# Optimization experiments

Measured on AMD Instinct MI355X. Metric: run time of the kernel, lower is better.

Reference implementation:

```python
import jax, jax.numpy as jnp
import numpy as np

N = 50000
E = 800000
IN_C = 128
HEADS = 2
OUT_C = 64
NEG_SLOPE = 0.2  # PyG GATConv leaky_relu slope


def setup_inputs() -> dict:
    key = jax.random.key(0)
    ks = jax.random.split(key, 12)
    glorot = lambda k, shape: jax.random.normal(k, shape, jnp.float32) * np.sqrt(2.0 / (shape[0] + shape[-1]))
    return {
        "node_h": jax.random.normal(ks[0], (N, IN_C), jnp.float32),
        "edge_index_pc": jax.random.randint(ks[1], (2, E), 0, N, jnp.int64),
        "edge_index_mc": jax.random.randint(ks[2], (2, E), 0, N, jnp.int64),
        "W_pc": glorot(ks[3], (IN_C, HEADS * OUT_C)),
        "att_src_pc": glorot(ks[4], (HEADS, OUT_C)),
        "att_dst_pc": glorot(ks[5], (HEADS, OUT_C)),
        "bias_pc": jnp.zeros((HEADS * OUT_C,), jnp.float32),
        "W_mc": glorot(ks[6], (IN_C, HEADS * OUT_C)),
        "att_src_mc": glorot(ks[7], (HEADS, OUT_C)),
        "att_dst_mc": glorot(ks[8], (HEADS, OUT_C)),
        "bias_mc": jnp.zeros((HEADS * OUT_C,), jnp.float32),
    }


def _gat_conv(x, edge_index, W, att_src, att_dst, bias):
    # PyG GATConv (concat=True). x: [N, in], edge_index: [2, E] (src -> dst).
    n = x.shape[0]
    H, C = att_src.shape
    xw = (x @ W).reshape(n, H, C)                      # [N, H, C]
    a_src = jnp.sum(xw * att_src, axis=-1)             # [N, H]
    a_dst = jnp.sum(xw * att_dst, axis=-1)             # [N, H]
    src, dst = edge_index[0], edge_index[1]
    e = jax.nn.leaky_relu(a_src[src] + a_dst[dst], negative_slope=NEG_SLOPE)  # [E, H]
    # segment softmax over edges sharing the same destination node
    m = jax.ops.segment_max(e, dst, num_segments=n)    # [N, H]
    m = jnp.where(jnp.isfinite(m), m, 0.0)             # guard isolated nodes
    ex = jnp.exp(e - m[dst])
    denom = jax.ops.segment_sum(ex, dst, num_segments=n)
    alpha = ex / (denom[dst] + 1e-16)                  # [E, H]
    msg = xw[src] * alpha[:, :, None]                  # [E, H, C]
    out = jax.ops.segment_sum(msg, dst, num_segments=n)  # [N, H, C]
    return out.reshape(n, H * C) + bias


def reference(node_h, edge_index_pc, edge_index_mc,
              W_pc, att_src_pc, att_dst_pc, bias_pc,
              W_mc, att_src_mc, att_dst_mc, bias_mc):
    # eval mode: F.dropout and GATConv attention dropout are identity
    h_pc = jax.nn.elu(_gat_conv(node_h, edge_index_pc, W_pc, att_src_pc, att_dst_pc, bias_pc))
    h_mc = jax.nn.elu(_gat_conv(node_h, edge_index_mc, W_mc, att_src_mc, att_dst_mc, bias_mc))
    return (h_pc + h_mc) * 0.5
```

## Files before the change

### kernel.cpp

```cpp
#include <hip/hip_runtime.h>
#include <hip/hip_bf16.h>

#define IN_C   128
#define HC     128
#define OUT_C  64
#define EPB    4096
#define NBMAX  1024
#define CAP    3072

typedef short bf16x8 __attribute__((ext_vector_type(8)));
typedef float f32x4  __attribute__((ext_vector_type(4)));

__device__ __forceinline__ unsigned short f2bf(float f) {
    unsigned u = __float_as_uint(f);
    return (unsigned short)((u + 0x7FFF + ((u >> 16) & 1)) >> 16);
}

__device__ __forceinline__ void fma8(float* acc, float al, uint4 v) {
    acc[0] += al * __uint_as_float(v.x << 16);
    acc[1] += al * __uint_as_float(v.x & 0xFFFF0000u);
    acc[2] += al * __uint_as_float(v.y << 16);
    acc[3] += al * __uint_as_float(v.y & 0xFFFF0000u);
    acc[4] += al * __uint_as_float(v.z << 16);
    acc[5] += al * __uint_as_float(v.z & 0xFFFF0000u);
    acc[6] += al * __uint_as_float(v.w << 16);
    acc[7] += al * __uint_as_float(v.w & 0xFFFF0000u);
}

__global__ void k_detect(const void* __restrict__ h,
                         const void* __restrict__ e1,
                         const void* __restrict__ e2,
                         int* __restrict__ flags)
{
    if (blockIdx.x == 0 && threadIdx.x == 0) {
        const unsigned short* u = (const unsigned short*)h;
        int f32 = 0;
        for (int k = 0; k < 512; ++k) {
            int ex = (u[k] >> 7) & 0xFF;
            if (ex >= 0xE0) { f32 = 1; break; }
        }
        flags[0] = f32;
        const int* a = (const int*)e1;
        const int* b = (const int*)e2;
        int any1 = 0, any2 = 0;
        for (int k = 0; k < 64; ++k) { any1 |= a[2*k+1]; any2 |= b[2*k+1]; }
        flags[1] = (any1 == 0);
        flags[2] = (any2 == 0);
        flags[3] = 0;
    }
}

__device__ __forceinline__ float ldf(const void* p, int i, int f32) {
    if (f32) return ((const float*)p)[i];
    return __bfloat162float(((const __hip_bfloat16*)p)[i]);
}

__device__ __forceinline__ void load_edge(const void* ei, int e, int E, int i64,
                                          int& s, int& d)
{
    if (i64) {
        s = (int)((const long long*)ei)[e];
        d = (int)((const long long*)ei)[E + e];
    } else {
        s = ((const int*)ei)[e];
        d = ((const int*)ei)[E + e];
    }
}

__global__ void k_fill_sentinel(float* out, int total, float v)
{
    int i = blockIdx.x * blockDim.x + threadIdx.x;
    if (i < total) out[i] = v;
}

__global__ __launch_bounds__(256)
void k_prep(const void* __restrict__ Wpc, const void* __restrict__ Wmc,
            const int* __restrict__ flags,
            unsigned short* __restrict__ WTpc, unsigned short* __restrict__ WTmc)
{
    int idx = blockIdx.x * 256 + threadIdx.x;
    if (idx >= 2 * IN_C * HC) return;
    int conv = idx >= IN_C * HC;
    int r = idx - conv * IN_C * HC;
    int k = r >> 7, j = r & 127;
    float v = ldf(conv ? Wmc : Wpc, r, flags[0]);
    (conv ? WTmc : WTpc)[(size_t)j * IN_C + k] = f2bf(v);
}

__global__ __launch_bounds__(256)
void k_gs(const void* __restrict__ h,
          const unsigned short* __restrict__ WT0,
          const unsigned short* __restrict__ WT1,
          const void* __restrict__ atS0, const void* __restrict__ atD0,
          const void* __restrict__ atS1, const void* __restrict__ atD1,
          const int* __restrict__ flags,
          unsigned short* __restrict__ xw0, unsigned short* __restrict__ xw1,
          float* __restrict__ oas0, float* __restrict__ oad0,
          float* __restrict__ oas1, float* __restrict__ oad1,
          int n, int blocksG,
          const void* __restrict__ e1, const void* __restrict__ e2, int E,
          int NB, int blocksB,
          int* __restrict__ gcur1, int* __restrict__ gcur2,
          unsigned* __restrict__ bkt1, unsigned* __restrict__ bkt2)
{
    __shared__ int sh[2 * NBMAX];
    int tid = threadIdx.x;

    if (blockIdx.y < 2) {
        if ((int)blockIdx.x >= blocksG) return;
        int conv = blockIdx.y;
        const unsigned short* WT = conv ? WT1 : WT0;
        const void* atS = conv ? atS1 : atS0;
        const void* atD = conv ? atD1 : atD0;
        unsigned short* xw = conv ? xw1 : xw0;
        float* oaS = conv ? oas1 : oas0;
        float* oaD = conv ? oad1 : oad0;

        int wave = tid >> 6, lane = tid & 63;
        int cl = lane & 15, grp = lane >> 4;
        int base = blockIdx.x * 64 + wave * 16;
        int f32 = flags[0];

        int nodeLoad = base + cl;
        int nl = nodeLoad < n ? nodeLoad : (n - 1);
        bf16x8 afr[4];
        #pragma unroll
        for (int s = 0; s < 4; ++s) {
            int k0 = 32 * s + 8 * grp;
            if (f32) {
                const float4* hr = (const float4*)((const float*)h + (size_t)nl * IN_C + k0);
                float4 u0 = hr[0], u1 = hr[1];
                afr[s][0] = (short)f2bf(u0.x); afr[s][1] = (short)f2bf(u0.y);
                afr[s][2] = (short)f2bf(u0.z); afr[s][3] = (short)f2bf(u0.w);
                afr[s][4] = (short)f2bf(u1.x); afr[s][5] = (short)f2bf(u1.y);
                afr[s][6] = (short)f2bf(u1.z); afr[s][7] = (short)f2bf(u1.w);
            } else {
                afr[s] = *(const bf16x8*)((const unsigned short*)h + (size_t)nl * IN_C + k0);
            }
        }

        float vs_[4][2] = {{0.f,0.f},{0.f,0.f},{0.f,0.f},{0.f,0.f}};
        float vd_[4][2] = {{0.f,0.f},{0.f,0.f},{0.f,0.f},{0.f,0.f}};

        #pragma unroll
        for (int t = 0; t < 8; ++t) {
            int col = t * 16 + cl;
            f32x4 acc = {0.f, 0.f, 0.f, 0.f};
            #pragma unroll
            for (int s = 0; s < 4; ++s) {
                int k0 = 32 * s + 8 * grp;
                bf16x8 b = *(const bf16x8*)(WT + (size_t)col * IN_C + k0);
                acc = __builtin_amdgcn_mfma_f32_16x16x32_bf16(afr[s], b, acc, 0, 0, 0);
            }
            float aS = ldf(atS, col, f32);
            float aD = ldf(atD, col, f32);
            int hd = t >> 2;
            #pragma unroll
            for (int r = 0; r < 4; ++r) {
                int nodeOut = base + 4 * grp + r;
                float v = acc[r];
                if (nodeOut < n) xw[(size_t)nodeOut * HC + col] = f2bf(v);
                vs_[r][hd] += v * aS;
                vd_[r][hd] += v * aD;
            }
        }
        #pragma unroll
        for (int r = 0; r < 4; ++r) {
            #pragma unroll
            for (int hd = 0; hd < 2; ++hd) {
                float vs = vs_[r][hd], vd = vd_[r][hd];
                #pragma unroll
                for (int off = 1; off < 16; off <<= 1) {
                    vs += __shfl_xor(vs, off);
                    vd += __shfl_xor(vd, off);
                }
                int nodeOut = base + 4 * grp + r;
                if (cl == 0 && nodeOut < n) {
                    oaS[nodeOut * 2 + hd] = vs;
                    oaD[nodeOut * 2 + hd] = vd;
                }
            }
        }
    } else {
        if ((int)blockIdx.x >= blocksB) return;
        int conv = blockIdx.y - 2;
        const void* ei = conv ? e2 : e1;
        int* gcur = conv ? gcur2 : gcur1;
        unsigned* bkt = conv ? bkt2 : bkt1;
        int* cnt = sh;
        int* lbase = sh + NBMAX;
        for (int i = tid; i < NB; i += 256) cnt[i] = 0;
        __syncthreads();
        int base = blockIdx.x * EPB;
        int i64 = flags[1 + conv];
        int ss[EPB / 256], dd[EPB / 256];
        #pragma unroll
        for (int k = 0; k < EPB / 256; ++k) {
            int e = base + k * 256 + tid;
            if (e < E) {
                int s, d; load_edge(ei, e, E, i64, s, d);
                ss[k] = s; dd[k] = d;
                atomicAdd(&cnt[d >> 7], 1);
            } else dd[k] = -1;
        }
        __syncthreads();
        for (int i = tid; i < NB; i += 256) {
            int c = cnt[i];
            lbase[i] = c ? atomicAdd(&gcur[i], c) : 0;
            cnt[i] = 0;
        }
        __syncthreads();
        #pragma unroll
        for (int k = 0; k < EPB / 256; ++k) {
            if (dd[k] >= 0) {
                int b = dd[k] >> 7;
                int pos = lbase[b] + atomicAdd(&cnt[b], 1);
                if (pos < CAP)
                    bkt[(size_t)b * CAP + pos] =
                        ((unsigned)(dd[k] & 127) << 17) | (unsigned)ss[k];
            }
        }
    }
}

__global__ __launch_bounds__(256)
void k_bcsr4(unsigned* __restrict__ bkt1, unsigned* __restrict__ bkt2,
             unsigned* __restrict__ alp1, unsigned* __restrict__ alp2,
             const int* __restrict__ gcur1, const int* __restrict__ gcur2,
             const float* __restrict__ as1, const float* __restrict__ ad1,
             const float* __restrict__ as2, const float* __restrict__ ad2,
             int2* __restrict__ rs1, int2* __restrict__ rs2,
             int NB, int n)
{
    __shared__ unsigned ebuf[CAP];
    __shared__ float sc0[CAP];
    __shared__ float sc1[CAP];
    __shared__ int cnt[128], off[128], exc[128];
    int conv = blockIdx.y;
    unsigned* seg = (conv ? bkt2 : bkt1) + (size_t)blockIdx.x * CAP;
    unsigned* alp = (conv ? alp2 : alp1) + (size_t)blockIdx.x * CAP;
    const int* gcur = conv ? gcur2 : gcur1;
    const float2* asv = (const float2*)(conv ? as2 : as1);
    const float2* adv = (const float2*)(conv ? ad2 : ad1);
    int2* rs = conv ? rs2 : rs1;
    int b = blockIdx.x, tid = threadIdx.x;
    int nb0 = b << 7;
    int nd = n - nb0; if (nd > 128) nd = 128;
    int cntE = gcur[b]; if (cntE > CAP) cntE = CAP;

    for (int i = tid; i < cntE; i += 256) ebuf[i] = seg[i];
    if (tid < 128) cnt[tid] = 0;
    __syncthreads();
    for (int i = tid; i < cntE; i += 256)
        atomicAdd(&cnt[ebuf[i] >> 17], 1);
    __syncthreads();
    int v = (tid < 128) ? cnt[tid] : 0;
    if (tid < 128) off[tid] = v;
    __syncthreads();
    for (int o = 1; o < 128; o <<= 1) {
        int x = (tid < 128 && tid >= o) ? off[tid - o] : 0;
        __syncthreads();
        if (tid < 128) off[tid] += x;
        __syncthreads();
    }
    if (tid < 128) exc[tid] = off[tid] - v;
    if (tid < nd) {
        int begA = b * CAP + exc[tid];
        rs[nb0 + tid] = make_int2(begA, begA + v);
    }
    if (tid < 128) cnt[tid] = 0;
    __syncthreads();
    for (int i = tid; i < cntE; i += 256) {
        unsigned pv = ebuf[i];
        int d = pv >> 17;
        int pos = atomicAdd(&cnt[d], 1);
        seg[exc[d] + pos] = pv & 0x1FFFFu;
    }
    __syncthreads();

    int d = tid >> 1, sub = tid & 1;
    int rc = (d < nd) ? cnt[d] : 0;
    int rb = exc[d];
    float2 ad = (d < nd) ? adv[nb0 + d] : make_float2(0.f, 0.f);
    float m0 = -1e30f, m1 = -1e30f;
    for (int i = sub; i < rc; i += 2) {
        int s = (int)seg[rb + i];
        float2 as = asv[s];
        float e0 = as.x + ad.x; e0 = e0 > 0.f ? e0 : 0.2f * e0;
        float e1 = as.y + ad.y; e1 = e1 > 0.f ? e1 : 0.2f * e1;
        sc0[rb + i] = e0; sc1[rb + i] = e1;
        m0 = fmaxf(m0, e0); m1 = fmaxf(m1, e1);
    }
    m0 = fmaxf(m0, __shfl_xor(m0, 1));
    m1 = fmaxf(m1, __shfl_xor(m1, 1));
    float s0 = 0.f, s1 = 0.f;
    for (int i = sub; i < rc; i += 2) {
        float ex0 = expf(sc0[rb + i] - m0);
        float ex1 = expf(sc1[rb + i] - m1);
        sc0[rb + i] = ex0; sc1[rb + i] = ex1;
        s0 += ex0; s1 += ex1;
    }
    s0 += __shfl_xor(s0, 1);
    s1 += __shfl_xor(s1, 1);
    float inv0 = 1.f / (s0 + 1e-16f), inv1 = 1.f / (s1 + 1e-16f);
    for (int i = sub; i < rc; i += 2) {
        unsigned a = (unsigned)f2bf(sc0[rb + i] * inv0)
                   | ((unsigned)f2bf(sc1[rb + i] * inv1) << 16);
        alp[rb + i] = a;
    }
}

__global__ __launch_bounds__(256)
void k_node11(const int2* __restrict__ rs1, const int2* __restrict__ rs2,
              const unsigned* __restrict__ csr1, const unsigned* __restrict__ csr2,
              const unsigned* __restrict__ alp1, const unsigned* __restrict__ alp2,
              const unsigned short* __restrict__ xw1, const unsigned short* __restrict__ xw2,
              const void* __restrict__ bias1, const void* __restrict__ bias2,
              const int* __restrict__ flags,
              float* __restrict__ out, int n)
{
    int tid = threadIdx.x;
    int nl = tid >> 4;
    int l  = tid & 15;
    int node = blockIdx.x * 16 + nl;
    if (node >= n) return;
    int f32 = flags[0];
    unsigned lofs = (unsigned)(l << 4);
    int c0 = l * 8;
    int hi = (l >= 8);
    float vv0[8];

    #pragma unroll
    for (int conv = 0; conv < 2; ++conv) {
        const int2* rs = conv ? rs2 : rs1;
        const unsigned* csr = conv ? csr2 : csr1;
        const unsigned* alp = conv ? alp2 : alp1;
        const char* xwb = (const char*)(conv ? xw2 : xw1);
        const void* bias = conv ? bias2 : bias1;

        int2 r = rs[node];
        int beg = r.x, deg = r.y - r.x;

        float acc[8] = {0.f,0.f,0.f,0.f,0.f,0.f,0.f,0.f};
        int t = 0;
        for (; t + 4 <= deg; t += 4) {
            unsigned sA = csr[beg + t],     sB = csr[beg + t + 1];
            unsigned sC = csr[beg + t + 2], sD = csr[beg + t + 3];
            unsigned aA = alp[beg + t],     aB = alp[beg + t + 1];
            unsigned aC = alp[beg + t + 2], aD = alp[beg + t + 3];
            uint4 vA = *(const uint4*)(xwb + (sA << 8) + lofs);
            uint4 vB = *(const uint4*)(xwb + (sB << 8) + lofs);
            uint4 vC = *(const uint4*)(xwb + (sC << 8) + lofs);
            uint4 vD = *(const uint4*)(xwb + (sD << 8) + lofs);
            float alA = __uint_as_float(hi ? (aA & 0xFFFF0000u) : (aA << 16));
            float alB = __uint_as_float(hi ? (aB & 0xFFFF0000u) : (aB << 16));
            float alC = __uint_as_float(hi ? (aC & 0xFFFF0000u) : (aC << 16));
            float alD = __uint_as_float(hi ? (aD & 0xFFFF0000u) : (aD << 16));
            fma8(acc, alA, vA);
            fma8(acc, alB, vB);
            fma8(acc, alC, vC);
            fma8(acc, alD, vD);
        }
        for (; t < deg; ++t) {
            unsigned s = csr[beg + t];
            unsigned a = alp[beg + t];
            float al = __uint_as_float(hi ? (a & 0xFFFF0000u) : (a << 16));
            uint4 v = *(const uint4*)(xwb + (s << 8) + lofs);
            fma8(acc, al, v);
        }

        if (conv == 0) {
            #pragma unroll
            for (int j = 0; j < 8; ++j) {
                float v = acc[j] + ldf(bias, c0 + j, f32);
                vv0[j] = v > 0.f ? v : expf(v) - 1.f;
            }
        } else {
            float vv1[8];
            #pragma unroll
            for (int j = 0; j < 8; ++j) {
                float v = acc[j] + ldf(bias, c0 + j, f32);
                vv1[j] = v > 0.f ? v : expf(v) - 1.f;
            }
            float4* o4 = (float4*)(out + (size_t)node * HC + c0);
            o4[0] = make_float4(0.5f * (vv0[0] + vv1[0]), 0.5f * (vv0[1] + vv1[1]),
                                0.5f * (vv0[2] + vv1[2]), 0.5f * (vv0[3] + vv1[3]));
            o4[1] = make_float4(0.5f * (vv0[4] + vv1[4]), 0.5f * (vv0[5] + vv1[5]),
                                0.5f * (vv0[6] + vv1[6]), 0.5f * (vv0[7] + vv1[7]));
        }
    }
}

static inline char* align64(char* p) {
    return (char*)(((size_t)p + 63) & ~(size_t)63);
}

extern "C" void kernel_launch(void* const* d_in, const int* in_sizes, int n_in,
                              void* d_out, int out_size, void* d_ws, size_t ws_size,
                              hipStream_t stream)
{
    const void* node_h = d_in[0];
    const void* ei_pc  = d_in[1];
    const void* ei_mc  = d_in[2];
    const void* W_pc   = d_in[3];
    const void* as_pc  = d_in[4];
    const void* ad_pc  = d_in[5];
    const void* b_pc   = d_in[6];
    const void* W_mc   = d_in[7];
    const void* as_mc  = d_in[8];
    const void* ad_mc  = d_in[9];
    const void* b_mc   = d_in[10];

    const int N = in_sizes[0] / IN_C;
    const int E = in_sizes[1] / 2;
    const int total = N * HC;
    const int NB = (N + 127) >> 7;
    float* out = (float*)d_out;
    const int fillBlocks = (out_size + 255) / 256;

    char* p = (char*)d_ws;
    int* flags = (int*)p;                       p += 256;
    unsigned short* WT_pc = (unsigned short*)p; p += (size_t)IN_C * HC * 2;
    unsigned short* WT_mc = (unsigned short*)p; p += (size_t)IN_C * HC * 2;
    unsigned short* xw_pc = (unsigned short*)p; p += (size_t)total * 2;
    unsigned short* xw_mc = (unsigned short*)p; p += (size_t)total * 2;
    float* aspc = (float*)p;                    p += (size_t)N * 2 * 4;
    float* adpc = (float*)p;                    p += (size_t)N * 2 * 4;
    float* asmc = (float*)p;                    p += (size_t)N * 2 * 4;
    float* admc = (float*)p;                    p += (size_t)N * 2 * 4;
    char* zbase = p;
    int* gcur1 = (int*)p;                       p += (size_t)NBMAX * 4;
    int* gcur2 = (int*)p;                       p += (size_t)NBMAX * 4;
    size_t zbytes = (size_t)(p - zbase);
    p = align64(p);
    int2* rs1 = (int2*)p;                       p += (size_t)N * 8;  p = align64(p);
    int2* rs2 = (int2*)p;                       p += (size_t)N * 8;  p = align64(p);
    unsigned* bkt1 = (unsigned*)p;              p += (size_t)NB * CAP * 4;
    unsigned* bkt2 = (unsigned*)p;              p += (size_t)NB * CAP * 4;
    unsigned* alp1 = (unsigned*)p;              p += (size_t)NB * CAP * 4;
    unsigned* alp2 = (unsigned*)p;              p += (size_t)NB * CAP * 4;

    {
        float sentinel = 0.f;
        if (n_in < 11) sentinel = 690.f;
        else if (in_sizes[1] != in_sizes[2]) sentinel = 702.f;
        else if (in_sizes[3] != IN_C * HC)   sentinel = 703.f;
        else if (in_sizes[7] != IN_C * HC)   sentinel = 707.f;
        else if (out_size != total)          sentinel = 720.f;
        else if (NB > NBMAX)                 sentinel = 730.f;
        else if (N >= (1 << 17))             sentinel = 741.f;
        size_t need = (size_t)(p - (char*)d_ws);
        if (sentinel == 0.f && ws_size < need) sentinel = 555.f;
        if (sentinel != 0.f) {
            k_fill_sentinel<<<fillBlocks, 256, 0, stream>>>(out, out_size, sentinel);
            return;
        }
    }

    k_detect<<<1, 64, 0, stream>>>(node_h, ei_pc, ei_mc, flags);
    k_prep<<<(2 * IN_C * HC + 255) / 256, 256, 0, stream>>>(W_pc, W_mc, flags, WT_pc, WT_mc);
    hipMemsetAsync(zbase, 0, zbytes, stream);

    const int blocksB = (E + EPB - 1) / EPB;
    const int blocksN = (N + 15) / 16;
    const int blocksG = (N + 63) / 64;
    const int gx = blocksG > blocksB ? blocksG : blocksB;

    k_gs<<<dim3(gx, 4), 256, 0, stream>>>(node_h, WT_pc, WT_mc,
                                          as_pc, ad_pc, as_mc, ad_mc, flags,
                                          xw_pc, xw_mc, aspc, adpc, asmc, admc,
                                          N, blocksG,
                                          ei_pc, ei_mc, E, NB, blocksB,
                                          gcur1, gcur2, bkt1, bkt2);

    k_bcsr4<<<dim3(NB, 2), 256, 0, stream>>>(bkt1, bkt2, alp1, alp2,
                                             gcur1, gcur2,
                                             aspc, adpc, asmc, admc,
                                             rs1, rs2, NB, N);

    k_node11<<<blocksN, 256, 0, stream>>>(rs1, rs2, bkt1, bkt2, alp1, alp2,
                                          xw_pc, xw_mc, b_pc, b_mc, flags,
                                          out, N);
}
```

Measured before the change: 154.4 us.

## Fuse edge-score softmax into scatter pass, dropping max subtraction

The per-destination softmax no longer runs as separate passes over shared-memory score arrays. Each thread computes the leaky-relu score and exp for its edges during the CSR scatter, accumulates per-node denominators with shared atomics, then normalizes from registers. Skipping the max subtraction removes a pass and 24KB of shared memory, which should raise occupancy. The cost is possible exp overflow if scores grow large, plus float-atomic contention and ordering nondeterminism in the sums.

New measurement: 160.3 us. 1.04x slower.

```diff
diff --git a/kernel.cpp b/kernel.cpp
--- a/kernel.cpp
+++ b/kernel.cpp
@@ -7,6 +7,7 @@
 #define EPB    4096
 #define NBMAX  1024
 #define CAP    3072
+#define NIT    (CAP / 256)
 
 typedef short bf16x8 __attribute__((ext_vector_type(8)));
 typedef float f32x4  __attribute__((ext_vector_type(4)));
@@ -224,7 +225,7 @@
 }
 
 __global__ __launch_bounds__(256)
-void k_bcsr4(unsigned* __restrict__ bkt1, unsigned* __restrict__ bkt2,
+void k_bcsr5(unsigned* __restrict__ bkt1, unsigned* __restrict__ bkt2,
              unsigned* __restrict__ alp1, unsigned* __restrict__ alp2,
              const int* __restrict__ gcur1, const int* __restrict__ gcur2,
              const float* __restrict__ as1, const float* __restrict__ ad1,
@@ -233,9 +234,8 @@
              int NB, int n)
 {
     __shared__ unsigned ebuf[CAP];
-    __shared__ float sc0[CAP];
-    __shared__ float sc1[CAP];
     __shared__ int cnt[128], off[128], exc[128];
+    __shared__ float dsum0[128], dsum1[128];
     int conv = blockIdx.y;
     unsigned* seg = (conv ? bkt2 : bkt1) + (size_t)blockIdx.x * CAP;
     unsigned* alp = (conv ? alp2 : alp1) + (size_t)blockIdx.x * CAP;
@@ -249,7 +249,7 @@
     int cntE = gcur[b]; if (cntE > CAP) cntE = CAP;
 
     for (int i = tid; i < cntE; i += 256) ebuf[i] = seg[i];
-    if (tid < 128) cnt[tid] = 0;
+    if (tid < 128) { cnt[tid] = 0; dsum0[tid] = 0.f; dsum1[tid] = 0.f; }
     __syncthreads();
     for (int i = tid; i < cntE; i += 256)
         atomicAdd(&cnt[ebuf[i] >> 17], 1);
@@ -270,43 +270,43 @@
     }
     if (tid < 128) cnt[tid] = 0;
     __syncthreads();
-    for (int i = tid; i < cntE; i += 256) {
-        unsigned pv = ebuf[i];
-        int d = pv >> 17;
-        int pos = atomicAdd(&cnt[d], 1);
-        seg[exc[d] + pos] = pv & 0x1FFFFu;
+
+    int   slot_[NIT];
+    int   dd_[NIT];
+    float ex0_[NIT], ex1_[NIT];
+    #pragma unroll
+    for (int k = 0; k < NIT; ++k) {
+        int i = k * 256 + tid;
+        slot_[k] = -1;
+        if (i < cntE) {
+            unsigned pv = ebuf[i];
+            int d = (int)(pv >> 17);
+            int src = (int)(pv & 0x1FFFFu);
+            float2 as = asv[src];
+            float2 ad = adv[nb0 + d];
+            float e0 = as.x + ad.x; e0 = e0 > 0.f ? e0 : 0.2f * e0;
+            float e1 = as.y + ad.y; e1 = e1 > 0.f ? e1 : 0.2f * e1;
+            float x0 = expf(e0), x1 = expf(e1);
+            int pos = atomicAdd(&cnt[d], 1);
+            int sl = exc[d] + pos;
+            seg[sl] = (unsigned)src;
+            atomicAdd(&dsum0[d], x0);
+            atomicAdd(&dsum1[d], x1);
+            slot_[k] = sl; dd_[k] = d; ex0_[k] = x0; ex1_[k] = x1;
+        }
     }
     __syncthreads();
 
-    int d = tid >> 1, sub = tid & 1;
-    int rc = (d < nd) ? cnt[d] : 0;
-    int rb = exc[d];
-    float2 ad = (d < nd) ? adv[nb0 + d] : make_float2(0.f, 0.f);
-    float m0 = -1e30f, m1 = -1e30f;
-    for (int i = sub; i < rc; i += 2) {
-        int s = (int)seg[rb + i];
-        float2 as = asv[s];
-        float e0 = as.x + ad.x; e0 = e0 > 0.f ? e0 : 0.2f * e0;
-        float e1 = as.y + ad.y; e1 = e1 > 0.f ? e1 : 0.2f * e1;
-        sc0[rb + i] = e0; sc1[rb + i] = e1;
-        m0 = fmaxf(m0, e0); m1 = fmaxf(m1, e1);
-    }
-    m0 = fmaxf(m0, __shfl_xor(m0, 1));
-    m1 = fmaxf(m1, __shfl_xor(m1, 1));
-    float s0 = 0.f, s1 = 0.f;
-    for (int i = sub; i < rc; i += 2) {
-        float ex0 = expf(sc0[rb + i] - m0);
-        float ex1 = expf(sc1[rb + i] - m1);
-        sc0[rb + i] = ex0; sc1[rb + i] = ex1;
-        s0 += ex0; s1 += ex1;
-    }
-    s0 += __shfl_xor(s0, 1);
-    s1 += __shfl_xor(s1, 1);
-    float inv0 = 1.f / (s0 + 1e-16f), inv1 = 1.f / (s1 + 1e-16f);
-    for (int i = sub; i < rc; i += 2) {
-        unsigned a = (unsigned)f2bf(sc0[rb + i] * inv0)
-                   | ((unsigned)f2bf(sc1[rb + i] * inv1) << 16);
-        alp[rb + i] = a;
+    #pragma unroll
+    for (int k = 0; k < NIT; ++k) {
+        if (slot_[k] >= 0) {
+            int d = dd_[k];
+            float i0 = 1.f / (dsum0[d] + 1e-16f);
+            float i1 = 1.f / (dsum1[d] + 1e-16f);
+            unsigned a = (unsigned)f2bf(ex0_[k] * i0)
+                       | ((unsigned)f2bf(ex1_[k] * i1) << 16);
+            alp[slot_[k]] = a;
+        }
     }
 }
 
@@ -473,7 +473,7 @@
                                           ei_pc, ei_mc, E, NB, blocksB,
                                           gcur1, gcur2, bkt1, bkt2);
 
-    k_bcsr4<<<dim3(NB, 2), 256, 0, stream>>>(bkt1, bkt2, alp1, alp2,
+    k_bcsr5<<<dim3(NB, 2), 256, 0, stream>>>(bkt1, bkt2, alp1, alp2,
                                              gcur1, gcur2,
                                              aspc, adpc, asmc, admc,
                                              rs1, rs2, NB, N);
```
